# Kernel tuning notes

Hardware: AMD Instinct MI355X
Metric: run time of the kernel (lower is better)

Reference implementation:

```python
import jax, jax.numpy as jnp
import numpy as np

H = 10  # hidden_dim

def _lstm_layer(x_tbd, w_ih, w_hh, b_ih, b_hh):
    # x_tbd: [T, B, D]; w_ih: [4H, D]; w_hh: [4H, H]; biases [4H]
    B = x_tbd.shape[1]
    h0 = jnp.zeros((B, H), x_tbd.dtype)
    c0 = jnp.zeros((B, H), x_tbd.dtype)
    # precompute input projections for all timesteps: [T, B, 4H]
    xg = jnp.einsum('tbd,gd->tbg', x_tbd, w_ih) + b_ih + b_hh

    def step(carry, xg_t):
        h, c = carry
        gates = xg_t + h @ w_hh.T  # [B, 4H]
        i, f, g, o = jnp.split(gates, 4, axis=-1)  # torch gate order i,f,g,o
        i = jax.nn.sigmoid(i); f = jax.nn.sigmoid(f)
        g = jnp.tanh(g); o = jax.nn.sigmoid(o)
        c = f * c + i * g
        h = o * jnp.tanh(c)
        return (h, c), h

    (hT, cT), hs = jax.lax.scan(step, (h0, c0), xg)
    return hs, hT  # hs: [T, B, H]

def setup_inputs() -> dict:
    key = jax.random.key(0)
    ks = jax.random.split(key, 11)
    B, T, D = 32768, 28, 28
    s0 = 1.0 / np.sqrt(H)
    u = lambda k, shape: jax.random.uniform(k, shape, jnp.float32, -s0, s0)
    return {
        'x': jax.random.normal(ks[0], (B, T, D), jnp.float32),
        'w_ih0': u(ks[1], (4 * H, D)),
        'w_hh0': u(ks[2], (4 * H, H)),
        'b_ih0': u(ks[3], (4 * H,)),
        'b_hh0': u(ks[4], (4 * H,)),
        'w_ih1': u(ks[5], (4 * H, H)),
        'w_hh1': u(ks[6], (4 * H, H)),
        'b_ih1': u(ks[7], (4 * H,)),
        'b_hh1': u(ks[8], (4 * H,)),
        'w_cls': u(ks[9], (10, H)),
        'b_cls': u(ks[10], (10,)),
    }

def reference(x, w_ih0, w_hh0, b_ih0, b_hh0, w_ih1, w_hh1, b_ih1, b_hh1, w_cls, b_cls):
    x_tbd = jnp.swapaxes(x, 0, 1)  # [T, B, D]
    hs0, _ = _lstm_layer(x_tbd, w_ih0, w_hh0, b_ih0, b_hh0)
    _, hT1 = _lstm_layer(hs0, w_ih1, w_hh1, b_ih1, b_hh1)  # hT1 = h_n[-1]
    return hT1 @ w_cls.T + b_cls  # [B, 10]
```

## Files before the change

### kernel.cpp

```cpp
#include <hip/hip_runtime.h>


#define HDIM 10
#define DDIM 28
#define TSTEPS 28

typedef __attribute__((ext_vector_type(8))) short short8;
typedef __attribute__((ext_vector_type(4))) float f32x4;

__device__ __forceinline__ unsigned short bf16_rne(float f) {
    unsigned u = __builtin_bit_cast(unsigned, f);
    u += 0x7FFFu + ((u >> 16) & 1u);
    return (unsigned short)(u >> 16);
}
__device__ __forceinline__ float bf16_f(unsigned short h) {
    unsigned u = ((unsigned)h) << 16;
    return __builtin_bit_cast(float, u);
}
__device__ __forceinline__ float act_eval(float v, float a) {
    return a * __builtin_amdgcn_rcpf(1.0f + __expf(-a * v)) + (1.0f - a);
}

#define FENCE() __asm volatile("" ::: "memory")

__global__ __launch_bounds__(64) void lstm2_mfma_kernel(
    const float* __restrict__ x,
    const float* __restrict__ w_ih0, const float* __restrict__ w_hh0,
    const float* __restrict__ b_ih0, const float* __restrict__ b_hh0,
    const float* __restrict__ w_ih1, const float* __restrict__ w_hh1,
    const float* __restrict__ b_ih1, const float* __restrict__ b_hh1,
    const float* __restrict__ w_cls, const float* __restrict__ b_cls,
    float* __restrict__ out)
{
    __shared__ unsigned short uA0[16 * 136];
    __shared__ unsigned short uA1[16 * 72];
    __shared__ float gbuf[48 * 20];
    __shared__ float hfin[16 * 12];

    const int l  = threadIdx.x;
    const int lm = l & 15;
    const int q  = l >> 4;
    const int sbase = blockIdx.x * 16;

    for (int i = l; i < 16 * 22; i += 64) uA0[(i / 22) * 136 + 114 + (i % 22)] = 0;
    for (int i = l; i < 16 * 12; i += 64) uA1[(i / 12) * 72 + 60 + (i % 12)] = 0;

    short8 B0[3][4], B1[3][2];
    #pragma unroll
    for (int T = 0; T < 3; ++T) {
        const int n = lm + 16 * T;
        #pragma unroll
        for (int c = 0; c < 4; ++c) {
            #pragma unroll
            for (int j = 0; j < 8; ++j) {
                const int kk = 32 * c + 8 * q + j;
                unsigned short bits = 0;
                if (n < 40 && kk < 114) {
                    int k2 = kk, want_lo = 0;
                    if (k2 >= 76)      { k2 -= 76; want_lo = 1; }
                    else if (k2 >= 38) { k2 -= 38; }
                    const float w = (k2 < 28) ? w_ih0[n * 28 + k2]
                                              : w_hh0[n * 10 + (k2 - 28)];
                    const unsigned short hi = bf16_rne(w);
                    bits = want_lo ? bf16_rne(w - bf16_f(hi)) : hi;
                }
                B0[T][c][j] = (short)bits;
            }
        }
        #pragma unroll
        for (int c = 0; c < 2; ++c) {
            #pragma unroll
            for (int j = 0; j < 8; ++j) {
                const int kk = 32 * c + 8 * q + j;
                unsigned short bits = 0;
                if (n < 40 && kk < 60) {
                    int k2 = kk, want_lo = 0;
                    if (k2 >= 40)      { k2 -= 40; want_lo = 1; }
                    else if (k2 >= 20) { k2 -= 20; }
                    const float w = (k2 < 10) ? w_ih1[n * 10 + k2]
                                              : w_hh1[n * 10 + (k2 - 10)];
                    const unsigned short hi = bf16_rne(w);
                    bits = want_lo ? bf16_rne(w - bf16_f(hi)) : hi;
                }
                B1[T][c][j] = (short)bits;
            }
        }
    }

    float bias0[3], bias1[3], aT[3];
    #pragma unroll
    for (int T = 0; T < 3; ++T) {
        const int n = lm + 16 * T;
        bias0[T] = (n < 40) ? (b_ih0[n] + b_hh0[n]) : 0.0f;
        bias1[T] = (n < 40) ? (b_ih1[n] + b_hh1[n]) : 0.0f;
        aT[T] = (n >= 20 && n < 30) ? 2.0f : 1.0f;
    }

    const float* xp[7]; int xsm[7], xd[7]; float xn[7];
    #pragma unroll
    for (int i = 0; i < 7; ++i) {
        const int f = l + 64 * i;
        const int sm = f / 28, d = f - 28 * sm;
        xsm[i] = sm; xd[i] = d;
        xp[i] = x + (size_t)(sbase + sm) * (TSTEPS * DDIM) + d;
        xn[i] = xp[i][0];
    }
    #pragma unroll
    for (int i = 0; i < 7; ++i) {
        const unsigned short hi = bf16_rne(xn[i]);
        const unsigned short lo = bf16_rne(xn[i] - bf16_f(hi));
        unsigned short* row = &uA0[xsm[i] * 136];
        row[xd[i]] = hi; row[38 + xd[i]] = lo; row[76 + xd[i]] = hi;
    }
    if (lm < 10) {
        #pragma unroll
        for (int r = 0; r < 4; ++r) {
            const int m = 4 * q + r;
            unsigned short* r0 = &uA0[m * 136];
            r0[28 + lm] = 0; r0[66 + lm] = 0; r0[104 + lm] = 0;
            unsigned short* r1 = &uA1[m * 72];
            r1[lm] = 0; r1[20 + lm] = 0; r1[40 + lm] = 0;
            r1[10 + lm] = 0; r1[30 + lm] = 0; r1[50 + lm] = 0;
        }
    }
    FENCE();

    float c0s[4] = {0, 0, 0, 0}, c1s[4] = {0, 0, 0, 0};
    float h1v[4] = {0, 0, 0, 0};

    #pragma unroll 1
    for (int t = 0; t < TSTEPS; ++t) {
        short8 A0[4];
        #pragma unroll
        for (int c = 0; c < 4; ++c)
            A0[c] = *(const short8*)&uA0[lm * 136 + 32 * c + 8 * q];
        FENCE();

        if (t + 1 < TSTEPS) {
            #pragma unroll
            for (int i = 0; i < 7; ++i) { xp[i] += DDIM; xn[i] = xp[i][0]; }
        }

        f32x4 C[3];
        #pragma unroll
        for (int T = 0; T < 3; ++T) {
            f32x4 acc = {bias0[T], bias0[T], bias0[T], bias0[T]};
            #pragma unroll
            for (int c = 0; c < 4; ++c)
                acc = __builtin_amdgcn_mfma_f32_16x16x32_bf16(A0[c], B0[T][c], acc, 0, 0, 0);
            C[T] = acc;
        }
        #pragma unroll
        for (int T = 0; T < 3; ++T) {
            const float a = aT[T];
            f32x4 gv;
            #pragma unroll
            for (int r = 0; r < 4; ++r) gv[r] = act_eval(C[T][r], a);
            *(f32x4*)&gbuf[(lm + 16 * T) * 20 + 4 * q] = gv;
        }
        FENCE();

        {
            const f32x4 iv = *(const f32x4*)&gbuf[(lm     ) * 20 + 4 * q];
            const f32x4 fv = *(const f32x4*)&gbuf[(lm + 10) * 20 + 4 * q];
            const f32x4 gg = *(const f32x4*)&gbuf[(lm + 20) * 20 + 4 * q];
            const f32x4 ov = *(const f32x4*)&gbuf[(lm + 30) * 20 + 4 * q];
            float h0v[4];
            #pragma unroll
            for (int r = 0; r < 4; ++r) {
                const float c = fv[r] * c0s[r] + iv[r] * gg[r];
                c0s[r] = c;
                h0v[r] = ov[r] * act_eval(c, 2.0f);
            }
            if (lm < 10) {
                #pragma unroll
                for (int r = 0; r < 4; ++r) {
                    const int m = 4 * q + r;
                    const unsigned short hi = bf16_rne(h0v[r]);
                    const unsigned short lo = bf16_rne(h0v[r] - bf16_f(hi));
                    unsigned short* r0 = &uA0[m * 136];
                    r0[28 + lm] = hi; r0[66 + lm] = lo; r0[104 + lm] = hi;
                    unsigned short* r1 = &uA1[m * 72];
                    r1[lm] = hi; r1[20 + lm] = lo; r1[40 + lm] = hi;
                }
            }
        }
        FENCE();

        short8 A1[2];
        #pragma unroll
        for (int c = 0; c < 2; ++c)
            A1[c] = *(const short8*)&uA1[lm * 72 + 32 * c + 8 * q];
        f32x4 D[3];
        #pragma unroll
        for (int T = 0; T < 3; ++T) {
            f32x4 acc = {bias1[T], bias1[T], bias1[T], bias1[T]};
            #pragma unroll
            for (int c = 0; c < 2; ++c)
                acc = __builtin_amdgcn_mfma_f32_16x16x32_bf16(A1[c], B1[T][c], acc, 0, 0, 0);
            D[T] = acc;
        }
        #pragma unroll
        for (int T = 0; T < 3; ++T) {
            const float a = aT[T];
            f32x4 gv;
            #pragma unroll
            for (int r = 0; r < 4; ++r) gv[r] = act_eval(D[T][r], a);
            *(f32x4*)&gbuf[(lm + 16 * T) * 20 + 4 * q] = gv;
        }
        FENCE();

        {
            const f32x4 iv = *(const f32x4*)&gbuf[(lm     ) * 20 + 4 * q];
            const f32x4 fv = *(const f32x4*)&gbuf[(lm + 10) * 20 + 4 * q];
            const f32x4 gg = *(const f32x4*)&gbuf[(lm + 20) * 20 + 4 * q];
            const f32x4 ov = *(const f32x4*)&gbuf[(lm + 30) * 20 + 4 * q];
            #pragma unroll
            for (int r = 0; r < 4; ++r) {
                const float c = fv[r] * c1s[r] + iv[r] * gg[r];
                c1s[r] = c;
                h1v[r] = ov[r] * act_eval(c, 2.0f);
            }
            if (lm < 10) {
                #pragma unroll
                for (int r = 0; r < 4; ++r) {
                    const int m = 4 * q + r;
                    const unsigned short hi = bf16_rne(h1v[r]);
                    const unsigned short lo = bf16_rne(h1v[r] - bf16_f(hi));
                    unsigned short* r1 = &uA1[m * 72];
                    r1[10 + lm] = hi; r1[30 + lm] = lo; r1[50 + lm] = hi;
                }
            }
        }
        FENCE();

        if (t + 1 < TSTEPS) {
            #pragma unroll
            for (int i = 0; i < 7; ++i) {
                const unsigned short hi = bf16_rne(xn[i]);
                const unsigned short lo = bf16_rne(xn[i] - bf16_f(hi));
                unsigned short* row = &uA0[xsm[i] * 136];
                row[xd[i]] = hi; row[38 + xd[i]] = lo; row[76 + xd[i]] = hi;
            }
        }
        FENCE();
    }

    if (lm < 10) {
        #pragma unroll
        for (int r = 0; r < 4; ++r) hfin[(4 * q + r) * 12 + lm] = h1v[r];
    }
    FENCE();
    if (lm < 10) {
        float wc[10];
        #pragma unroll
        for (int j = 0; j < 10; ++j) wc[j] = w_cls[lm * 10 + j];
        const float bo = b_cls[lm];
        #pragma unroll
        for (int r = 0; r < 4; ++r) {
            const int m = 4 * q + r;
            float acc = bo;
            #pragma unroll
            for (int j = 0; j < 10; ++j) acc += hfin[m * 12 + j] * wc[j];
            out[(size_t)(sbase + m) * 10 + lm] = acc;
        }
    }
}

extern "C" void kernel_launch(void* const* d_in, const int* in_sizes, int n_in,
                              void* d_out, int out_size, void* d_ws, size_t ws_size,
                              hipStream_t stream) {
    const float* x     = (const float*)d_in[0];
    const float* w_ih0 = (const float*)d_in[1];
    const float* w_hh0 = (const float*)d_in[2];
    const float* b_ih0 = (const float*)d_in[3];
    const float* b_hh0 = (const float*)d_in[4];
    const float* w_ih1 = (const float*)d_in[5];
    const float* w_hh1 = (const float*)d_in[6];
    const float* b_ih1 = (const float*)d_in[7];
    const float* b_hh1 = (const float*)d_in[8];
    const float* w_cls = (const float*)d_in[9];
    const float* b_cls = (const float*)d_in[10];
    float* out = (float*)d_out;

    const int B = in_sizes[0] / (TSTEPS * DDIM);
    const int grid = B / 16;

    hipLaunchKernelGGL(lstm2_mfma_kernel, dim3(grid), dim3(64), 0, stream,
                       x, w_ih0, w_hh0, b_ih0, b_hh0,
                       w_ih1, w_hh1, b_ih1, b_hh1,
                       w_cls, b_cls, out);
}
```

Baseline: 265.7 us.

## Skew layer-1 LSTM one step behind layer 0 to interleave both layers per iteration

```diff
diff --git a/kernel.cpp b/kernel.cpp
--- a/kernel.cpp
+++ b/kernel.cpp
@@ -34,7 +34,8 @@
 {
     __shared__ unsigned short uA0[16 * 136];
     __shared__ unsigned short uA1[16 * 72];
-    __shared__ float gbuf[48 * 20];
+    __shared__ float gbuf0[48 * 20];
+    __shared__ float gbuf1[48 * 20];
     __shared__ float hfin[16 * 12];
 
     const int l  = threadIdx.x;
@@ -96,21 +97,20 @@
         aT[T] = (n >= 20 && n < 30) ? 2.0f : 1.0f;
     }
 
-    const float* xp[7]; int xsm[7], xd[7]; float xn[7];
+    int xoff[7], lofs[7]; float xn[7];
     #pragma unroll
     for (int i = 0; i < 7; ++i) {
         const int f = l + 64 * i;
         const int sm = f / 28, d = f - 28 * sm;
-        xsm[i] = sm; xd[i] = d;
-        xp[i] = x + (size_t)(sbase + sm) * (TSTEPS * DDIM) + d;
-        xn[i] = xp[i][0];
+        lofs[i] = sm * 136 + d;
+        xoff[i] = (sbase + sm) * (TSTEPS * DDIM) + d;
+        xn[i] = x[xoff[i]];
     }
     #pragma unroll
     for (int i = 0; i < 7; ++i) {
         const unsigned short hi = bf16_rne(xn[i]);
         const unsigned short lo = bf16_rne(xn[i] - bf16_f(hi));
-        unsigned short* row = &uA0[xsm[i] * 136];
-        row[xd[i]] = hi; row[38 + xd[i]] = lo; row[76 + xd[i]] = hi;
+        uA0[lofs[i]] = hi; uA0[lofs[i] + 38] = lo; uA0[lofs[i] + 76] = hi;
     }
     if (lm < 10) {
         #pragma unroll
@@ -127,123 +127,187 @@
 
     float c0s[4] = {0, 0, 0, 0}, c1s[4] = {0, 0, 0, 0};
     float h1v[4] = {0, 0, 0, 0};
+    float h0v[4];
+    short8 A0f[4], A1f[2];
+
+    #pragma unroll
+    for (int c = 0; c < 4; ++c)
+        A0f[c] = *(const short8*)&uA0[lm * 136 + 32 * c + 8 * q];
+    FENCE();
+    #pragma unroll
+    for (int i = 0; i < 7; ++i) { xoff[i] += DDIM; xn[i] = x[xoff[i]]; }
+    {
+        f32x4 C[3];
+        #pragma unroll
+        for (int T = 0; T < 3; ++T) {
+            f32x4 acc = {bias0[T], bias0[T], bias0[T], bias0[T]};
+            #pragma unroll
+            for (int c = 0; c < 4; ++c)
+                acc = __builtin_amdgcn_mfma_f32_16x16x32_bf16(A0f[c], B0[T][c], acc, 0, 0, 0);
+            C[T] = acc;
+        }
+        #pragma unroll
+        for (int T = 0; T < 3; ++T) {
+            f32x4 gv;
+            #pragma unroll
+            for (int r = 0; r < 4; ++r) gv[r] = act_eval(C[T][r], aT[T]);
+            *(f32x4*)&gbuf0[(lm + 16 * T) * 20 + 4 * q] = gv;
+        }
+    }
+    FENCE();
+    {
+        const f32x4 iv = *(const f32x4*)&gbuf0[(lm     ) * 20 + 4 * q];
+        const f32x4 fv = *(const f32x4*)&gbuf0[(lm + 10) * 20 + 4 * q];
+        const f32x4 gg = *(const f32x4*)&gbuf0[(lm + 20) * 20 + 4 * q];
+        const f32x4 ov = *(const f32x4*)&gbuf0[(lm + 30) * 20 + 4 * q];
+        #pragma unroll
+        for (int r = 0; r < 4; ++r) {
+            const float c = fv[r] * c0s[r] + iv[r] * gg[r];
+            c0s[r] = c;
+            h0v[r] = ov[r] * act_eval(c, 2.0f);
+        }
+        if (lm < 10) {
+            #pragma unroll
+            for (int r = 0; r < 4; ++r) {
+                const int m = 4 * q + r;
+                const unsigned short hi = bf16_rne(h0v[r]);
+                const unsigned short lo = bf16_rne(h0v[r] - bf16_f(hi));
+                unsigned short* r0 = &uA0[m * 136];
+                r0[28 + lm] = hi; r0[66 + lm] = lo; r0[104 + lm] = hi;
+                unsigned short* r1 = &uA1[m * 72];
+                r1[lm] = hi; r1[20 + lm] = lo; r1[40 + lm] = hi;
+            }
+        }
+    }
+    FENCE();
+    #pragma unroll
+    for (int i = 0; i < 7; ++i) {
+        const unsigned short hi = bf16_rne(xn[i]);
+        const unsigned short lo = bf16_rne(xn[i] - bf16_f(hi));
+        uA0[lofs[i]] = hi; uA0[lofs[i] + 38] = lo; uA0[lofs[i] + 76] = hi;
+    }
+    FENCE();
 
     #pragma unroll 1
-    for (int t = 0; t < TSTEPS; ++t) {
-        short8 A0[4];
+    for (int t = 0; t < TSTEPS - 1; ++t) {
+        #pragma unroll
+        for (int c = 0; c < 2; ++c)
+            A1f[c] = *(const short8*)&uA1[lm * 72 + 32 * c + 8 * q];
         #pragma unroll
         for (int c = 0; c < 4; ++c)
-            A0[c] = *(const short8*)&uA0[lm * 136 + 32 * c + 8 * q];
-        FENCE();
-
-        if (t + 1 < TSTEPS) {
-            #pragma unroll
-            for (int i = 0; i < 7; ++i) { xp[i] += DDIM; xn[i] = xp[i][0]; }
-        }
-
-        f32x4 C[3];
-        #pragma unroll
-        for (int T = 0; T < 3; ++T) {
-            f32x4 acc = {bias0[T], bias0[T], bias0[T], bias0[T]};
+            A0f[c] = *(const short8*)&uA0[lm * 136 + 32 * c + 8 * q];
+        FENCE();
+
+        if (t < TSTEPS - 2) {
+            #pragma unroll
+            for (int i = 0; i < 7; ++i) { xoff[i] += DDIM; xn[i] = x[xoff[i]]; }
+        }
+
+        f32x4 C[3], D[3];
+        #pragma unroll
+        for (int T = 0; T < 3; ++T) {
+            f32x4 accD = {bias1[T], bias1[T], bias1[T], bias1[T]};
+            #pragma unroll
+            for (int c = 0; c < 2; ++c)
+                accD = __builtin_amdgcn_mfma_f32_16x16x32_bf16(A1f[c], B1[T][c], accD, 0, 0, 0);
+            D[T] = accD;
+            f32x4 accC = {bias0[T], bias0[T], bias0[T], bias0[T]};
             #pragma unroll
             for (int c = 0; c < 4; ++c)
-                acc = __builtin_amdgcn_mfma_f32_16x16x32_bf16(A0[c], B0[T][c], acc, 0, 0, 0);
-            C[T] = acc;
-        }
-        #pragma unroll
-        for (int T = 0; T < 3; ++T) {
-            const float a = aT[T];
-            f32x4 gv;
-            #pragma unroll
-            for (int r = 0; r < 4; ++r) gv[r] = act_eval(C[T][r], a);
-            *(f32x4*)&gbuf[(lm + 16 * T) * 20 + 4 * q] = gv;
+                accC = __builtin_amdgcn_mfma_f32_16x16x32_bf16(A0f[c], B0[T][c], accC, 0, 0, 0);
+            C[T] = accC;
+        }
+
+        #pragma unroll
+        for (int T = 0; T < 3; ++T) {
+            f32x4 gv1, gv0;
+            #pragma unroll
+            for (int r = 0; r < 4; ++r) {
+                gv1[r] = act_eval(D[T][r], aT[T]);
+                gv0[r] = act_eval(C[T][r], aT[T]);
+            }
+            *(f32x4*)&gbuf1[(lm + 16 * T) * 20 + 4 * q] = gv1;
+            *(f32x4*)&gbuf0[(lm + 16 * T) * 20 + 4 * q] = gv0;
         }
         FENCE();
 
         {
-            const f32x4 iv = *(const f32x4*)&gbuf[(lm     ) * 20 + 4 * q];
-            const f32x4 fv = *(const f32x4*)&gbuf[(lm + 10) * 20 + 4 * q];
-            const f32x4 gg = *(const f32x4*)&gbuf[(lm + 20) * 20 + 4 * q];
-            const f32x4 ov = *(const f32x4*)&gbuf[(lm + 30) * 20 + 4 * q];
-            float h0v[4];
+            const f32x4 iv1 = *(const f32x4*)&gbuf1[(lm     ) * 20 + 4 * q];
+            const f32x4 fv1 = *(const f32x4*)&gbuf1[(lm + 10) * 20 + 4 * q];
+            const f32x4 gg1 = *(const f32x4*)&gbuf1[(lm + 20) * 20 + 4 * q];
+            const f32x4 ov1 = *(const f32x4*)&gbuf1[(lm + 30) * 20 + 4 * q];
+            const f32x4 iv0 = *(const f32x4*)&gbuf0[(lm     ) * 20 + 4 * q];
+            const f32x4 fv0 = *(const f32x4*)&gbuf0[(lm + 10) * 20 + 4 * q];
+            const f32x4 gg0 = *(const f32x4*)&gbuf0[(lm + 20) * 20 + 4 * q];
+            const f32x4 ov0 = *(const f32x4*)&gbuf0[(lm + 30) * 20 + 4 * q];
             #pragma unroll
             for (int r = 0; r < 4; ++r) {
-                const float c = fv[r] * c0s[r] + iv[r] * gg[r];
-                c0s[r] = c;
-                h0v[r] = ov[r] * act_eval(c, 2.0f);
+                const float c1 = fv1[r] * c1s[r] + iv1[r] * gg1[r];
+                c1s[r] = c1;
+                h1v[r] = ov1[r] * act_eval(c1, 2.0f);
+                const float c0 = fv0[r] * c0s[r] + iv0[r] * gg0[r];
+                c0s[r] = c0;
+                h0v[r] = ov0[r] * act_eval(c0, 2.0f);
             }
             if (lm < 10) {
                 #pragma unroll
                 for (int r = 0; r < 4; ++r) {
                     const int m = 4 * q + r;
-                    const unsigned short hi = bf16_rne(h0v[r]);
-                    const unsigned short lo = bf16_rne(h0v[r] - bf16_f(hi));
+                    const unsigned short hi1 = bf16_rne(h1v[r]);
+                    const unsigned short lo1 = bf16_rne(h1v[r] - bf16_f(hi1));
+                    unsigned short* r1 = &uA1[m * 72];
+                    r1[10 + lm] = hi1; r1[30 + lm] = lo1; r1[50 + lm] = hi1;
+                    const unsigned short hi0 = bf16_rne(h0v[r]);
+                    const unsigned short lo0 = bf16_rne(h0v[r] - bf16_f(hi0));
                     unsigned short* r0 = &uA0[m * 136];
-                    r0[28 + lm] = hi; r0[66 + lm] = lo; r0[104 + lm] = hi;
-                    unsigned short* r1 = &uA1[m * 72];
-                    r1[lm] = hi; r1[20 + lm] = lo; r1[40 + lm] = hi;
+                    r0[28 + lm] = hi0; r0[66 + lm] = lo0; r0[104 + lm] = hi0;
+                    r1[lm] = hi0; r1[20 + lm] = lo0; r1[40 + lm] = hi0;
                 }
             }
         }
         FENCE();
 
-        short8 A1[2];
-        #pragma unroll
-        for (int c = 0; c < 2; ++c)
-            A1[c] = *(const short8*)&uA1[lm * 72 + 32 * c + 8 * q];
-        f32x4 D[3];
-        #pragma unroll
-        for (int T = 0; T < 3; ++T) {
-            f32x4 acc = {bias1[T], bias1[T], bias1[T], bias1[T]};
-            #pragma unroll
-            for (int c = 0; c < 2; ++c)
-                acc = __builtin_amdgcn_mfma_f32_16x16x32_bf16(A1[c], B1[T][c], acc, 0, 0, 0);
-            D[T] = acc;
-        }
-        #pragma unroll
-        for (int T = 0; T < 3; ++T) {
-            const float a = aT[T];
-            f32x4 gv;
-            #pragma unroll
-            for (int r = 0; r < 4; ++r) gv[r] = act_eval(D[T][r], a);
-            *(f32x4*)&gbuf[(lm + 16 * T) * 20 + 4 * q] = gv;
-        }
-        FENCE();
-
-        {
-            const f32x4 iv = *(const f32x4*)&gbuf[(lm     ) * 20 + 4 * q];
-            const f32x4 fv = *(const f32x4*)&gbuf[(lm + 10) * 20 + 4 * q];
-            const f32x4 gg = *(const f32x4*)&gbuf[(lm + 20) * 20 + 4 * q];
-            const f32x4 ov = *(const f32x4*)&gbuf[(lm + 30) * 20 + 4 * q];
-            #pragma unroll
-            for (int r = 0; r < 4; ++r) {
-                const float c = fv[r] * c1s[r] + iv[r] * gg[r];
-                c1s[r] = c;
-                h1v[r] = ov[r] * act_eval(c, 2.0f);
-            }
-            if (lm < 10) {
-                #pragma unroll
-                for (int r = 0; r < 4; ++r) {
-                    const int m = 4 * q + r;
-                    const unsigned short hi = bf16_rne(h1v[r]);
-                    const unsigned short lo = bf16_rne(h1v[r] - bf16_f(hi));
-                    unsigned short* r1 = &uA1[m * 72];
-                    r1[10 + lm] = hi; r1[30 + lm] = lo; r1[50 + lm] = hi;
-                }
-            }
-        }
-        FENCE();
-
-        if (t + 1 < TSTEPS) {
+        if (t < TSTEPS - 2) {
             #pragma unroll
             for (int i = 0; i < 7; ++i) {
                 const unsigned short hi = bf16_rne(xn[i]);
                 const unsigned short lo = bf16_rne(xn[i] - bf16_f(hi));
-                unsigned short* row = &uA0[xsm[i] * 136];
-                row[xd[i]] = hi; row[38 + xd[i]] = lo; row[76 + xd[i]] = hi;
-            }
-        }
-        FENCE();
+                uA0[lofs[i]] = hi; uA0[lofs[i] + 38] = lo; uA0[lofs[i] + 76] = hi;
+            }
+        }
+        FENCE();
+    }
+
+    {
+        #pragma unroll
+        for (int c = 0; c < 2; ++c)
+            A1f[c] = *(const short8*)&uA1[lm * 72 + 32 * c + 8 * q];
+        f32x4 D[3];
+        #pragma unroll
+        for (int T = 0; T < 3; ++T) {
+            f32x4 acc = {bias1[T], bias1[T], bias1[T], bias1[T]};
+            #pragma unroll
+            for (int c = 0; c < 2; ++c)
+                acc = __builtin_amdgcn_mfma_f32_16x16x32_bf16(A1f[c], B1[T][c], acc, 0, 0, 0);
+            D[T] = acc;
+        }
+        #pragma unroll
+        for (int T = 0; T < 3; ++T) {
+            f32x4 gv;
+            #pragma unroll
+            for (int r = 0; r < 4; ++r) gv[r] = act_eval(D[T][r], aT[T]);
+            *(f32x4*)&gbuf1[(lm + 16 * T) * 20 + 4 * q] = gv;
+        }
+        FENCE();
+        const f32x4 iv = *(const f32x4*)&gbuf1[(lm     ) * 20 + 4 * q];
+        const f32x4 fv = *(const f32x4*)&gbuf1[(lm + 10) * 20 + 4 * q];
+        const f32x4 gg = *(const f32x4*)&gbuf1[(lm + 20) * 20 + 4 * q];
+        const f32x4 ov = *(const f32x4*)&gbuf1[(lm + 30) * 20 + 4 * q];
+        #pragma unroll
+        for (int r = 0; r < 4; ++r) {
+            const float c = fv[r] * c1s[r] + iv[r] * gg[r];
+            h1v[r] = ov[r] * act_eval(c, 2.0f);
+        }
     }
 
     if (lm < 10) {
```

Result: faster. 259.9 us (-2.2%).
